# Performance work log

Measured on AMD Instinct MI355X. Metric: run time of the kernel, lower is better.

Reference implementation:

```python
import jax, jax.numpy as jnp
import numpy as np

B, H, S, D = 1, 16, 4096, 64


def setup_inputs() -> dict:
    key = jax.random.key(0)
    kq, kk, kv, km = jax.random.split(key, 4)
    q = jax.random.normal(kq, (B, H, S, D), dtype=jnp.float32)
    k = jax.random.normal(kk, (B, H, S, D), dtype=jnp.float32)
    v = jax.random.normal(kv, (B, H, S, D), dtype=jnp.float32)
    # bool mask, True = masked out (broadcasts over batch and heads)
    mask = jax.random.randint(km, (1, 1, S, S), 0, 2).astype(jnp.bool_)
    return {"q": q, "k": k, "v": v, "mask": mask}


def reference(q, k, v, mask):
    head_dim = q.shape[-1]
    scale = 1.0 / jnp.sqrt(jnp.asarray(head_dim, dtype=q.dtype))
    # [B,H,S,S] score matrix (the unfused form this module implements)
    scores = jnp.einsum("bhqd,bhkd->bhqk", q, k) * scale
    scores = jnp.where(mask, jnp.asarray(-jnp.inf, dtype=scores.dtype), scores)
    attn = jax.nn.softmax(scores, axis=-1)
    out = jnp.einsum("bhqk,bhkd->bhqd", attn, v)
    return (out, attn)
```

## Files before the change

kernel.cpp:

```cpp
#include <hip/hip_runtime.h>
#include <hip/hip_fp16.h>

namespace {
constexpr int S  = 4096;
constexpr int D  = 64;
constexpr int NH = 16;
constexpr int SW = S / 64;
constexpr float kScaleLog2e = 0.125f * 1.44269504088896340736f;

typedef _Float16 f16x8 __attribute__((ext_vector_type(8)));
typedef float    f32x4 __attribute__((ext_vector_type(4)));

__device__ inline f32x4 mfma16(f16x8 a, f16x8 b, f32x4 c) {
  return __builtin_amdgcn_mfma_f32_16x16x32_f16(a, b, c, 0, 0, 0);
}

__device__ inline void cvt_store(_Float16* dst, const float4 f) {
  union { ushort4 u; _Float16 h4[4]; } cv;
  cv.h4[0] = (_Float16)f.x; cv.h4[1] = (_Float16)f.y;
  cv.h4[2] = (_Float16)f.z; cv.h4[3] = (_Float16)f.w;
  *(ushort4*)dst = cv.u;
}
}

__global__ void pack_mask(const int* __restrict__ mask, unsigned long long* __restrict__ bits) {
  const int lane = threadIdx.x & 63;
  const int wid  = (int)((blockIdx.x * blockDim.x + threadIdx.x) >> 6);
  const int nwv  = (int)((gridDim.x * blockDim.x) >> 6);
  for (int w = wid; w < S * S / 64; w += nwv) {
    const int mv = mask[(size_t)w * 64 + lane];
    const unsigned long long b = __ballot(mv != 0);
    if (lane == 0) bits[w] = b;
  }
}

template<bool USE_BITS>
__global__ __launch_bounds__(256, 4)
void sdpa_kernel(const float* __restrict__ q, const float* __restrict__ k,
                 const float* __restrict__ v, const int* __restrict__ mask,
                 const unsigned long long* __restrict__ mbits,
                 float* __restrict__ out, float* __restrict__ attn)
{
  __shared__ _Float16 Qs[64][72];
  __shared__ _Float16 KV[2][64][72];
  __shared__ _Float16 Ps[4][16][72];

  const int tid  = threadIdx.x;
  const int wave = tid >> 6;
  const int lane = tid & 63;
  const int quad = lane >> 4;
  const int l16  = lane & 15;

  const int bid = (int)blockIdx.x;
  const int swz = (bid & 7) * 128 + (bid >> 3);
  const int h   = swz >> 6;
  const int q0  = (swz & 63) * 64;

  const float* __restrict__ qh = q + (size_t)h * S * D;
  const float* __restrict__ kh = k + (size_t)h * S * D;
  const float* __restrict__ vh = v + (size_t)h * S * D;

  #pragma unroll
  for (int t = 0; t < 4; ++t) {
    const int i   = tid + t * 256;
    const int row = i >> 4;
    const int c4  = i & 15;
    const float4 f = *(const float4*)(qh + (size_t)(q0 + row) * D + c4 * 4);
    cvt_store(&Qs[row][c4 * 4], f);
  }
  __syncthreads();

  const f16x8 qa0 = *(const f16x8*)&Qs[wave * 16 + l16][quad * 8];
  const f16x8 qa1 = *(const f16x8*)&Qs[wave * 16 + l16][32 + quad * 8];

  const int mrow0 = q0 + wave * 16 + quad * 4;

  float4 kf[4];
  #pragma unroll
  for (int t = 0; t < 4; ++t) {
    const int i = tid + t * 256;
    kf[t] = *(const float4*)(kh + (size_t)(i >> 4) * D + (i & 15) * 4);
  }
  #pragma unroll
  for (int t = 0; t < 4; ++t) {
    const int i = tid + t * 256;
    cvt_store(&KV[0][i >> 4][(i & 15) * 4], kf[t]);
  }
  __syncthreads();

  float lsum[4] = {0.f, 0.f, 0.f, 0.f};

  for (int kt = 0; kt < 64; ++kt) {
    const int cur = kt & 1;
    if (kt < 63) {
      const float* __restrict__ src = kh + (size_t)(kt + 1) * 64 * D;
      #pragma unroll
      for (int t = 0; t < 4; ++t) {
        const int i = tid + t * 256;
        kf[t] = *(const float4*)(src + (size_t)(i >> 4) * D + (i & 15) * 4);
      }
    }
    unsigned long long mw[4];
    if constexpr (USE_BITS) {
      #pragma unroll
      for (int r = 0; r < 4; ++r) mw[r] = mbits[(size_t)(mrow0 + r) * SW + kt];
    }

    #pragma unroll
    for (int nt = 0; nt < 4; ++nt) {
      const f16x8 kb0 = *(const f16x8*)&KV[cur][nt * 16 + l16][quad * 8];
      const f16x8 kb1 = *(const f16x8*)&KV[cur][nt * 16 + l16][32 + quad * 8];
      f32x4 acc = {0.f, 0.f, 0.f, 0.f};
      acc = mfma16(qa0, kb0, acc);
      acc = mfma16(qa1, kb1, acc);
      #pragma unroll
      for (int r = 0; r < 4; ++r) {
        bool masked;
        if constexpr (USE_BITS) {
          masked = ((unsigned)(mw[r] >> (nt * 16)) >> l16) & 1u;
        } else {
          masked = mask[(size_t)(mrow0 + r) * S + (kt * 64 + nt * 16 + l16)] != 0;
        }
        const float p = masked ? 0.0f : exp2f(acc[r] * kScaleLog2e);
        lsum[r] += p;
      }
    }

    if (kt < 63) {
      #pragma unroll
      for (int t = 0; t < 4; ++t) {
        const int i = tid + t * 256;
        cvt_store(&KV[cur ^ 1][i >> 4][(i & 15) * 4], kf[t]);
      }
    }
    __syncthreads();
  }

  float rinv[4];
  #pragma unroll
  for (int r = 0; r < 4; ++r) {
    float s = lsum[r];
    s += __shfl_xor(s, 1);
    s += __shfl_xor(s, 2);
    s += __shfl_xor(s, 4);
    s += __shfl_xor(s, 8);
    rinv[r] = 1.0f / s;
  }

  f32x4 Of[4];
  #pragma unroll
  for (int dt = 0; dt < 4; ++dt) Of[dt] = (f32x4){0.f, 0.f, 0.f, 0.f};

  float* __restrict__ attn_h = attn + (size_t)h * S * S;

  #pragma unroll
  for (int t = 0; t < 4; ++t) {
    const int i = tid + t * 256;
    kf[t] = *(const float4*)(kh + (size_t)(i >> 4) * D + (i & 15) * 4);
  }

  for (int kt = 0; kt < 64; ++kt) {
    const int kk0 = kt * 64;
    float4 vf[4];
    #pragma unroll
    for (int t = 0; t < 4; ++t) {
      const int i = tid + t * 256;
      const int n = i & 63;
      const int c = i >> 6;
      vf[t] = *(const float4*)(vh + (size_t)(kk0 + n) * D + c * 4);
    }
    unsigned long long mw[4];
    if constexpr (USE_BITS) {
      #pragma unroll
      for (int r = 0; r < 4; ++r) mw[r] = mbits[(size_t)(mrow0 + r) * SW + kt];
    }
    __syncthreads();

    #pragma unroll
    for (int t = 0; t < 4; ++t) {
      const int i = tid + t * 256;
      cvt_store(&KV[0][i >> 4][(i & 15) * 4], kf[t]);
    }
    #pragma unroll
    for (int t = 0; t < 4; ++t) {
      const int i = tid + t * 256;
      const int n = i & 63;
      const int c = i >> 6;
      KV[1][c * 4 + 0][n] = (_Float16)vf[t].x;
      KV[1][c * 4 + 1][n] = (_Float16)vf[t].y;
      KV[1][c * 4 + 2][n] = (_Float16)vf[t].z;
      KV[1][c * 4 + 3][n] = (_Float16)vf[t].w;
    }
    if (kt < 63) {
      const float* __restrict__ src = kh + (size_t)(kt + 1) * 64 * D;
      #pragma unroll
      for (int t = 0; t < 4; ++t) {
        const int i = tid + t * 256;
        kf[t] = *(const float4*)(src + (size_t)(i >> 4) * D + (i & 15) * 4);
      }
    }
    __syncthreads();

    #pragma unroll
    for (int nt = 0; nt < 4; ++nt) {
      const f16x8 kb0 = *(const f16x8*)&KV[0][nt * 16 + l16][quad * 8];
      const f16x8 kb1 = *(const f16x8*)&KV[0][nt * 16 + l16][32 + quad * 8];
      f32x4 acc = {0.f, 0.f, 0.f, 0.f};
      acc = mfma16(qa0, kb0, acc);
      acc = mfma16(qa1, kb1, acc);
      const int col = kk0 + nt * 16 + l16;
      #pragma unroll
      for (int r = 0; r < 4; ++r) {
        bool masked;
        if constexpr (USE_BITS) {
          masked = ((unsigned)(mw[r] >> (nt * 16)) >> l16) & 1u;
        } else {
          masked = mask[(size_t)(mrow0 + r) * S + col] != 0;
        }
        const float p = masked ? 0.0f : exp2f(acc[r] * kScaleLog2e) * rinv[r];
        __builtin_nontemporal_store(p, &attn_h[(size_t)(mrow0 + r) * S + col]);
        Ps[wave][quad * 4 + r][nt * 16 + l16] = (_Float16)p;
      }
    }

    const f16x8 pa0 = *(const f16x8*)&Ps[wave][l16][quad * 8];
    const f16x8 pa1 = *(const f16x8*)&Ps[wave][l16][32 + quad * 8];
    __builtin_amdgcn_s_setprio(1);
    #pragma unroll
    for (int dt = 0; dt < 4; ++dt) {
      const f16x8 vb0 = *(const f16x8*)&KV[1][dt * 16 + l16][quad * 8];
      const f16x8 vb1 = *(const f16x8*)&KV[1][dt * 16 + l16][32 + quad * 8];
      Of[dt] = mfma16(pa0, vb0, Of[dt]);
      Of[dt] = mfma16(pa1, vb1, Of[dt]);
    }
    __builtin_amdgcn_s_setprio(0);
  }

  #pragma unroll
  for (int dt = 0; dt < 4; ++dt)
    #pragma unroll
    for (int r = 0; r < 4; ++r)
      __builtin_nontemporal_store(Of[dt][r],
          &out[((size_t)h * S + (mrow0 + r)) * D + dt * 16 + l16]);
}

extern "C" void kernel_launch(void* const* d_in, const int* in_sizes, int n_in,
                              void* d_out, int out_size, void* d_ws, size_t ws_size,
                              hipStream_t stream) {
  const float* q    = (const float*)d_in[0];
  const float* k    = (const float*)d_in[1];
  const float* v    = (const float*)d_in[2];
  const int*   mask = (const int*)d_in[3];
  float* out  = (float*)d_out;
  float* attn = out + (size_t)NH * S * D;

  const size_t need = (size_t)S * (size_t)S / 8;
  if (d_ws != nullptr && ws_size >= need) {
    unsigned long long* mbits = (unsigned long long*)d_ws;
    pack_mask<<<dim3(1024), 256, 0, stream>>>(mask, mbits);
    sdpa_kernel<true><<<dim3(1024), 256, 0, stream>>>(q, k, v, mask, mbits, out, attn);
  } else {
    sdpa_kernel<false><<<dim3(1024), 256, 0, stream>>>(q, k, v, mask, nullptr, out, attn);
  }
}
```

Measured before the change: 1.512 ms.

## Compute attention in one pass with deferred row normalization via a rescale kernel

Replaces the two-pass scheme, which recomputed QK^T and exp once for row sums and again for probabilities, with a single pass. That pass writes unnormalized exp scores to attn, accumulates P·V, and normalizes the output by the row sum at the end. A separate rescale kernel then reads the whole attn matrix back and multiplies each row by its stored inverse sum. V loads are now prefetched alongside K in the single loop. The change removes a full QK^T/exp sweep but adds an extra read and write of the large attn tensor.

```diff
diff --git a/kernel.cpp b/kernel.cpp
--- a/kernel.cpp
+++ b/kernel.cpp
@@ -34,15 +34,35 @@
   }
 }
 
-template<bool USE_BITS>
+__global__ __launch_bounds__(256)
+void rescale_attn(float* __restrict__ attn, const float* __restrict__ rinv) {
+  const int tid = threadIdx.x;
+  const int h   = blockIdx.y;
+  const int r0  = blockIdx.x * 8;
+  #pragma unroll
+  for (int r8 = 0; r8 < 8; ++r8) {
+    const float sc = rinv[(size_t)h * S + r0 + r8];
+    f32x4* p = (f32x4*)(attn + ((size_t)h * S + r0 + r8) * S);
+    #pragma unroll
+    for (int u = 0; u < 4; ++u) {
+      const int j = tid + u * 256;
+      f32x4 x = __builtin_nontemporal_load(p + j);
+      x *= sc;
+      __builtin_nontemporal_store(x, p + j);
+    }
+  }
+}
+
 __global__ __launch_bounds__(256, 4)
-void sdpa_kernel(const float* __restrict__ q, const float* __restrict__ k,
-                 const float* __restrict__ v, const int* __restrict__ mask,
-                 const unsigned long long* __restrict__ mbits,
-                 float* __restrict__ out, float* __restrict__ attn)
+void sdpa_onepass(const float* __restrict__ q, const float* __restrict__ k,
+                  const float* __restrict__ v,
+                  const unsigned long long* __restrict__ mbits,
+                  float* __restrict__ out, float* __restrict__ attn,
+                  float* __restrict__ rinv_out)
 {
   __shared__ _Float16 Qs[64][72];
-  __shared__ _Float16 KV[2][64][72];
+  __shared__ _Float16 Ks[64][72];
+  __shared__ _Float16 Vts[64][72];
   __shared__ _Float16 Ps[4][16][72];
 
   const int tid  = threadIdx.x;
@@ -75,65 +95,81 @@
 
   const int mrow0 = q0 + wave * 16 + quad * 4;
 
-  float4 kf[4];
+  float4 kf[4], vf[4];
   #pragma unroll
   for (int t = 0; t < 4; ++t) {
     const int i = tid + t * 256;
     kf[t] = *(const float4*)(kh + (size_t)(i >> 4) * D + (i & 15) * 4);
-  }
-  #pragma unroll
-  for (int t = 0; t < 4; ++t) {
-    const int i = tid + t * 256;
-    cvt_store(&KV[0][i >> 4][(i & 15) * 4], kf[t]);
-  }
-  __syncthreads();
+    vf[t] = *(const float4*)(vh + (size_t)(i & 63) * D + (i >> 6) * 4);
+  }
 
   float lsum[4] = {0.f, 0.f, 0.f, 0.f};
+  f32x4 Of[4];
+  #pragma unroll
+  for (int dt = 0; dt < 4; ++dt) Of[dt] = (f32x4){0.f, 0.f, 0.f, 0.f};
+
+  float* __restrict__ attn_h = attn + (size_t)h * S * S;
 
   for (int kt = 0; kt < 64; ++kt) {
-    const int cur = kt & 1;
+    __syncthreads();
+
+    #pragma unroll
+    for (int t = 0; t < 4; ++t) {
+      const int i = tid + t * 256;
+      cvt_store(&Ks[i >> 4][(i & 15) * 4], kf[t]);
+      const int n = i & 63;
+      const int c = i >> 6;
+      Vts[c * 4 + 0][n] = (_Float16)vf[t].x;
+      Vts[c * 4 + 1][n] = (_Float16)vf[t].y;
+      Vts[c * 4 + 2][n] = (_Float16)vf[t].z;
+      Vts[c * 4 + 3][n] = (_Float16)vf[t].w;
+    }
     if (kt < 63) {
-      const float* __restrict__ src = kh + (size_t)(kt + 1) * 64 * D;
+      const float* __restrict__ ksrc = kh + (size_t)(kt + 1) * 64 * D;
+      const float* __restrict__ vsrc = vh + (size_t)(kt + 1) * 64 * D;
       #pragma unroll
       for (int t = 0; t < 4; ++t) {
         const int i = tid + t * 256;
-        kf[t] = *(const float4*)(src + (size_t)(i >> 4) * D + (i & 15) * 4);
+        kf[t] = *(const float4*)(ksrc + (size_t)(i >> 4) * D + (i & 15) * 4);
+        vf[t] = *(const float4*)(vsrc + (size_t)(i & 63) * D + (i >> 6) * 4);
       }
     }
     unsigned long long mw[4];
-    if constexpr (USE_BITS) {
-      #pragma unroll
-      for (int r = 0; r < 4; ++r) mw[r] = mbits[(size_t)(mrow0 + r) * SW + kt];
-    }
-
+    #pragma unroll
+    for (int r = 0; r < 4; ++r) mw[r] = mbits[(size_t)(mrow0 + r) * SW + kt];
+
+    __syncthreads();
+
+    const int kk0 = kt * 64;
     #pragma unroll
     for (int nt = 0; nt < 4; ++nt) {
-      const f16x8 kb0 = *(const f16x8*)&KV[cur][nt * 16 + l16][quad * 8];
-      const f16x8 kb1 = *(const f16x8*)&KV[cur][nt * 16 + l16][32 + quad * 8];
+      const f16x8 kb0 = *(const f16x8*)&Ks[nt * 16 + l16][quad * 8];
+      const f16x8 kb1 = *(const f16x8*)&Ks[nt * 16 + l16][32 + quad * 8];
       f32x4 acc = {0.f, 0.f, 0.f, 0.f};
       acc = mfma16(qa0, kb0, acc);
       acc = mfma16(qa1, kb1, acc);
+      const int col = kk0 + nt * 16 + l16;
       #pragma unroll
       for (int r = 0; r < 4; ++r) {
-        bool masked;
-        if constexpr (USE_BITS) {
-          masked = ((unsigned)(mw[r] >> (nt * 16)) >> l16) & 1u;
-        } else {
-          masked = mask[(size_t)(mrow0 + r) * S + (kt * 64 + nt * 16 + l16)] != 0;
-        }
+        const bool masked = ((unsigned)(mw[r] >> (nt * 16)) >> l16) & 1u;
         const float p = masked ? 0.0f : exp2f(acc[r] * kScaleLog2e);
+        __builtin_nontemporal_store(p, &attn_h[(size_t)(mrow0 + r) * S + col]);
         lsum[r] += p;
-      }
-    }
-
-    if (kt < 63) {
-      #pragma unroll
-      for (int t = 0; t < 4; ++t) {
-        const int i = tid + t * 256;
-        cvt_store(&KV[cur ^ 1][i >> 4][(i & 15) * 4], kf[t]);
-      }
-    }
-    __syncthreads();
+        Ps[wave][quad * 4 + r][nt * 16 + l16] = (_Float16)p;
+      }
+    }
+
+    const f16x8 pa0 = *(const f16x8*)&Ps[wave][l16][quad * 8];
+    const f16x8 pa1 = *(const f16x8*)&Ps[wave][l16][32 + quad * 8];
+    __builtin_amdgcn_s_setprio(1);
+    #pragma unroll
+    for (int dt = 0; dt < 4; ++dt) {
+      const f16x8 vb0 = *(const f16x8*)&Vts[dt * 16 + l16][quad * 8];
+      const f16x8 vb1 = *(const f16x8*)&Vts[dt * 16 + l16][32 + quad * 8];
+      Of[dt] = mfma16(pa0, vb0, Of[dt]);
+      Of[dt] = mfma16(pa1, vb1, Of[dt]);
+    }
+    __builtin_amdgcn_s_setprio(0);
   }
 
   float rinv[4];
@@ -146,11 +182,114 @@
     s += __shfl_xor(s, 8);
     rinv[r] = 1.0f / s;
   }
+  if (l16 == 0) {
+    #pragma unroll
+    for (int r = 0; r < 4; ++r) rinv_out[(size_t)h * S + mrow0 + r] = rinv[r];
+  }
+
+  #pragma unroll
+  for (int dt = 0; dt < 4; ++dt)
+    #pragma unroll
+    for (int r = 0; r < 4; ++r)
+      __builtin_nontemporal_store(Of[dt][r] * rinv[r],
+          &out[((size_t)h * S + (mrow0 + r)) * D + dt * 16 + l16]);
+}
+
+__global__ __launch_bounds__(256, 4)
+void sdpa_twopass(const float* __restrict__ q, const float* __restrict__ k,
+                  const float* __restrict__ v, const int* __restrict__ mask,
+                  float* __restrict__ out, float* __restrict__ attn)
+{
+  __shared__ _Float16 Qs[64][72];
+  __shared__ _Float16 KV[2][64][72];
+  __shared__ _Float16 Ps[4][16][72];
+
+  const int tid  = threadIdx.x;
+  const int wave = tid >> 6;
+  const int lane = tid & 63;
+  const int quad = lane >> 4;
+  const int l16  = lane & 15;
+
+  const int bid = (int)blockIdx.x;
+  const int swz = (bid & 7) * 128 + (bid >> 3);
+  const int h   = swz >> 6;
+  const int q0  = (swz & 63) * 64;
+
+  const float* __restrict__ qh = q + (size_t)h * S * D;
+  const float* __restrict__ kh = k + (size_t)h * S * D;
+  const float* __restrict__ vh = v + (size_t)h * S * D;
+
+  #pragma unroll
+  for (int t = 0; t < 4; ++t) {
+    const int i   = tid + t * 256;
+    const float4 f = *(const float4*)(qh + (size_t)(q0 + (i >> 4)) * D + (i & 15) * 4);
+    cvt_store(&Qs[i >> 4][(i & 15) * 4], f);
+  }
+  __syncthreads();
+
+  const f16x8 qa0 = *(const f16x8*)&Qs[wave * 16 + l16][quad * 8];
+  const f16x8 qa1 = *(const f16x8*)&Qs[wave * 16 + l16][32 + quad * 8];
+  const int mrow0 = q0 + wave * 16 + quad * 4;
+
+  float4 kf[4];
+  #pragma unroll
+  for (int t = 0; t < 4; ++t) {
+    const int i = tid + t * 256;
+    kf[t] = *(const float4*)(kh + (size_t)(i >> 4) * D + (i & 15) * 4);
+  }
+  #pragma unroll
+  for (int t = 0; t < 4; ++t) {
+    const int i = tid + t * 256;
+    cvt_store(&KV[0][i >> 4][(i & 15) * 4], kf[t]);
+  }
+  __syncthreads();
+
+  float lsum[4] = {0.f, 0.f, 0.f, 0.f};
+  for (int kt = 0; kt < 64; ++kt) {
+    const int cur = kt & 1;
+    if (kt < 63) {
+      const float* __restrict__ src = kh + (size_t)(kt + 1) * 64 * D;
+      #pragma unroll
+      for (int t = 0; t < 4; ++t) {
+        const int i = tid + t * 256;
+        kf[t] = *(const float4*)(src + (size_t)(i >> 4) * D + (i & 15) * 4);
+      }
+    }
+    #pragma unroll
+    for (int nt = 0; nt < 4; ++nt) {
+      const f16x8 kb0 = *(const f16x8*)&KV[cur][nt * 16 + l16][quad * 8];
+      const f16x8 kb1 = *(const f16x8*)&KV[cur][nt * 16 + l16][32 + quad * 8];
+      f32x4 acc = {0.f, 0.f, 0.f, 0.f};
+      acc = mfma16(qa0, kb0, acc);
+      acc = mfma16(qa1, kb1, acc);
+      #pragma unroll
+      for (int r = 0; r < 4; ++r) {
+        const int mv = mask[(size_t)(mrow0 + r) * S + (kt * 64 + nt * 16 + l16)];
+        lsum[r] += mv ? 0.0f : exp2f(acc[r] * kScaleLog2e);
+      }
+    }
+    if (kt < 63) {
+      #pragma unroll
+      for (int t = 0; t < 4; ++t) {
+        const int i = tid + t * 256;
+        cvt_store(&KV[cur ^ 1][i >> 4][(i & 15) * 4], kf[t]);
+      }
+    }
+    __syncthreads();
+  }
+
+  float rinv[4];
+  #pragma unroll
+  for (int r = 0; r < 4; ++r) {
+    float s = lsum[r];
+    s += __shfl_xor(s, 1); s += __shfl_xor(s, 2);
+    s += __shfl_xor(s, 4); s += __shfl_xor(s, 8);
+    rinv[r] = 1.0f / s;
+  }
 
   f32x4 Of[4];
   #pragma unroll
   for (int dt = 0; dt < 4; ++dt) Of[dt] = (f32x4){0.f, 0.f, 0.f, 0.f};
-
   float* __restrict__ attn_h = attn + (size_t)h * S * S;
 
   #pragma unroll
@@ -165,25 +304,13 @@
     #pragma unroll
     for (int t = 0; t < 4; ++t) {
       const int i = tid + t * 256;
-      const int n = i & 63;
-      const int c = i >> 6;
-      vf[t] = *(const float4*)(vh + (size_t)(kk0 + n) * D + c * 4);
-    }
-    unsigned long long mw[4];
-    if constexpr (USE_BITS) {
-      #pragma unroll
-      for (int r = 0; r < 4; ++r) mw[r] = mbits[(size_t)(mrow0 + r) * SW + kt];
-    }
-    __syncthreads();
-
+      vf[t] = *(const float4*)(vh + (size_t)(kk0 + (i & 63)) * D + (i >> 6) * 4);
+    }
+    __syncthreads();
     #pragma unroll
     for (int t = 0; t < 4; ++t) {
       const int i = tid + t * 256;
       cvt_store(&KV[0][i >> 4][(i & 15) * 4], kf[t]);
-    }
-    #pragma unroll
-    for (int t = 0; t < 4; ++t) {
-      const int i = tid + t * 256;
       const int n = i & 63;
       const int c = i >> 6;
       KV[1][c * 4 + 0][n] = (_Float16)vf[t].x;
@@ -211,21 +338,14 @@
       const int col = kk0 + nt * 16 + l16;
       #pragma unroll
       for (int r = 0; r < 4; ++r) {
-        bool masked;
-        if constexpr (USE_BITS) {
-          masked = ((unsigned)(mw[r] >> (nt * 16)) >> l16) & 1u;
-        } else {
-          masked = mask[(size_t)(mrow0 + r) * S + col] != 0;
-        }
-        const float p = masked ? 0.0f : exp2f(acc[r] * kScaleLog2e) * rinv[r];
+        const int mv = mask[(size_t)(mrow0 + r) * S + col];
+        const float p = mv ? 0.0f : exp2f(acc[r] * kScaleLog2e) * rinv[r];
         __builtin_nontemporal_store(p, &attn_h[(size_t)(mrow0 + r) * S + col]);
         Ps[wave][quad * 4 + r][nt * 16 + l16] = (_Float16)p;
       }
     }
-
     const f16x8 pa0 = *(const f16x8*)&Ps[wave][l16][quad * 8];
     const f16x8 pa1 = *(const f16x8*)&Ps[wave][l16][32 + quad * 8];
-    __builtin_amdgcn_s_setprio(1);
     #pragma unroll
     for (int dt = 0; dt < 4; ++dt) {
       const f16x8 vb0 = *(const f16x8*)&KV[1][dt * 16 + l16][quad * 8];
@@ -233,9 +353,7 @@
       Of[dt] = mfma16(pa0, vb0, Of[dt]);
       Of[dt] = mfma16(pa1, vb1, Of[dt]);
     }
-    __builtin_amdgcn_s_setprio(0);
-  }
-
+  }
   #pragma unroll
   for (int dt = 0; dt < 4; ++dt)
     #pragma unroll
@@ -254,12 +372,15 @@
   float* out  = (float*)d_out;
   float* attn = out + (size_t)NH * S * D;
 
-  const size_t need = (size_t)S * (size_t)S / 8;
-  if (d_ws != nullptr && ws_size >= need) {
+  const size_t bits_bytes = (size_t)S * (size_t)S / 8;
+  const size_t rinv_bytes = (size_t)NH * (size_t)S * 4;
+  if (d_ws != nullptr && ws_size >= bits_bytes + rinv_bytes) {
     unsigned long long* mbits = (unsigned long long*)d_ws;
+    float* rinv = (float*)((char*)d_ws + bits_bytes);
     pack_mask<<<dim3(1024), 256, 0, stream>>>(mask, mbits);
-    sdpa_kernel<true><<<dim3(1024), 256, 0, stream>>>(q, k, v, mask, mbits, out, attn);
+    sdpa_onepass<<<dim3(1024), 256, 0, stream>>>(q, k, v, mbits, out, attn, rinv);
+    rescale_attn<<<dim3(S / 8, NH), 256, 0, stream>>>(attn, rinv);
   } else {
-    sdpa_kernel<false><<<dim3(1024), 256, 0, stream>>>(q, k, v, mask, nullptr, out, attn);
-  }
-}
+    sdpa_twopass<<<dim3(1024), 256, 0, stream>>>(q, k, v, mask, out, attn);
+  }
+}
```

New measurement: 1.921 ms. 27.0% more time.
